# Optimization experiments

Hardware: AMD Instinct MI355X
Metric: run time of the kernel (lower is better)

Reference implementation:

```python
import jax, jax.numpy as jnp
import numpy as np

NEG_SLOPE = 0.2  # PyG GATConv default LeakyReLU slope
BN_EPS = 1e-5


def gat_layer(x, src, dst, W, a_src, a_dst, num_nodes):
    """PyG-style GATConv (no dropout, eval mode). Returns [N, H, C]."""
    H, C = a_src.shape
    h = (x @ W).reshape(-1, H, C)                       # [N,H,C]
    s_src = jnp.einsum('nhc,hc->nh', h, a_src)          # [N,H]
    s_dst = jnp.einsum('nhc,hc->nh', h, a_dst)          # [N,H]
    e = jax.nn.leaky_relu(s_src[src] + s_dst[dst], NEG_SLOPE)  # [E,H]
    # segment softmax over incoming edges of each dst node
    e_max = jax.ops.segment_max(e, dst, num_segments=num_nodes)  # [N,H]
    e_exp = jnp.exp(e - e_max[dst])
    denom = jax.ops.segment_sum(e_exp, dst, num_segments=num_nodes)
    alpha = e_exp / (denom[dst] + 1e-16)                # [E,H]
    msg = h[src] * alpha[:, :, None]                    # [E,H,C] (dominant intermediate)
    return jax.ops.segment_sum(msg, dst, num_segments=num_nodes)  # [N,H,C]


def setup_inputs() -> dict:
    key = jax.random.key(0)
    ks = jax.random.split(key, 12)
    N, Din, Hdim, Heads, Dout = 50000, 128, 128, 8, 128
    E = 150000
    inp = {}
    inp['x'] = jax.random.normal(ks[0], (N, Din), dtype=jnp.float32)
    inp['edge_index'] = jax.random.randint(ks[1], (2, E), 0, N, dtype=jnp.int64)
    sc1 = 1.0 / np.sqrt(Din)
    inp['W1'] = jax.random.uniform(ks[2], (Din, Heads * Hdim), minval=-sc1, maxval=sc1, dtype=jnp.float32)
    inp['a_src1'] = jax.random.normal(ks[3], (Heads, Hdim), dtype=jnp.float32) * 0.1
    inp['a_dst1'] = jax.random.normal(ks[4], (Heads, Hdim), dtype=jnp.float32) * 0.1
    inp['b1'] = jnp.zeros((Heads * Hdim,), dtype=jnp.float32)
    inp['gamma'] = jnp.ones((Heads * Hdim,), dtype=jnp.float32)
    inp['beta'] = jnp.zeros((Heads * Hdim,), dtype=jnp.float32)
    sc2 = 1.0 / np.sqrt(Heads * Hdim)
    inp['W2'] = jax.random.uniform(ks[5], (Heads * Hdim, Dout), minval=-sc2, maxval=sc2, dtype=jnp.float32)
    inp['a_src2'] = jax.random.normal(ks[6], (1, Dout), dtype=jnp.float32) * 0.1
    inp['a_dst2'] = jax.random.normal(ks[7], (1, Dout), dtype=jnp.float32) * 0.1
    inp['b2'] = jnp.zeros((Dout,), dtype=jnp.float32)
    return inp


def reference(x, W1, a_src1, a_dst1, b1, gamma, beta, W2, a_src2, a_dst2, b2, edge_index):
    N = x.shape[0]
    src, dst = edge_index[0], edge_index[1]
    # GAT layer 1: heads=8, concat=True
    h1 = gat_layer(x, src, dst, W1, a_src1, a_dst1, N)   # [N,8,128]
    h1 = h1.reshape(N, -1) + b1                          # [N,1024]
    # BatchNorm1d (training-mode batch stats, biased variance as in torch)
    mu = jnp.mean(h1, axis=0)
    var = jnp.var(h1, axis=0)
    h1 = gamma * (h1 - mu) * jax.lax.rsqrt(var + BN_EPS) + beta
    h1 = jax.nn.elu(h1)
    # GAT layer 2: heads=1, concat=False (mean == squeeze for 1 head)
    h2 = gat_layer(h1, src, dst, W2, a_src2, a_dst2, N)  # [N,1,128]
    return h2[:, 0, :] + b2
```

## Files before the change

kernel.cpp:

```cpp
#include <hip/hip_runtime.h>
#include <hip/hip_bf16.h>
#include <math.h>

#define NEG_SLOPE 0.2f
#define BN_EPS 1e-5f

typedef short bf16x8 __attribute__((ext_vector_type(8)));
typedef float f32x4 __attribute__((ext_vector_type(4)));

__device__ __forceinline__ float bf2f(unsigned short u) {
  union { unsigned int i; float f; } v;
  v.i = ((unsigned int)u) << 16;
  return v.f;
}
__device__ __forceinline__ unsigned short f2bf(float f) {
  union { unsigned int i; float f; } v;
  v.f = f;
  unsigned int i = v.i;
  unsigned int r = (i + 0x7fffu + ((i >> 16) & 1u)) >> 16;
  return (unsigned short)r;
}

__global__ __launch_bounds__(256) void detect_kernel(
    const unsigned int* __restrict__ xw, const unsigned int* __restrict__ eiw,
    int E, int* __restrict__ flags) {
  __shared__ int cnt[2];
  if (threadIdx.x < 2) cnt[threadIdx.x] = 0;
  __syncthreads();
  int t = threadIdx.x;
  int inrange = 0;
  for (int i = t; i < 2048; i += 256) {
    unsigned int e = (xw[i] >> 7) & 0xFFu;
    inrange += (e >= 100u && e <= 135u) ? 1 : 0;
  }
  atomicAdd(&cnt[0], inrange);
  int M = min(1024, E / 2);
  int zeros = 0;
  for (int i = t; i < M; i += 256) zeros += (eiw[2 * i + 1] == 0u) ? 1 : 0;
  atomicAdd(&cnt[1], zeros);
  __syncthreads();
  if (t == 0) {
    flags[0] = (cnt[0] > 1536) ? 1 : 0;
    flags[1] = (cnt[1] > M / 2) ? 1 : 0;
  }
}

__global__ __launch_bounds__(256) void canon_x8(
    const void* __restrict__ src, unsigned short* __restrict__ dst, int n_real,
    int n_total, const int* __restrict__ flags) {
  int i = (blockIdx.x * 256 + threadIdx.x) * 8;
  if (i >= n_total) return;
  union { bf16x8 v; unsigned short u[8]; } o;
  if (i < n_real) {
    if (flags[0]) {
      o.v = *(const bf16x8*)((const unsigned short*)src + i);
    } else {
      const float4* f = (const float4*)((const float*)src + i);
      float4 f0 = f[0];
      float4 f1 = f[1];
      o.u[0] = f2bf(f0.x); o.u[1] = f2bf(f0.y);
      o.u[2] = f2bf(f0.z); o.u[3] = f2bf(f0.w);
      o.u[4] = f2bf(f1.x); o.u[5] = f2bf(f1.y);
      o.u[6] = f2bf(f1.z); o.u[7] = f2bf(f1.w);
    }
  } else {
#pragma unroll
    for (int j = 0; j < 8; ++j) o.u[j] = 0;
  }
  *(bf16x8*)(dst + i) = o.v;
}

__global__ __launch_bounds__(256) void canon_w_t(
    const void* __restrict__ src, unsigned short* __restrict__ dst, int Kdim,
    int Ndim, const int* __restrict__ flags) {
  int i = blockIdx.x * 256 + threadIdx.x;
  if (i >= Kdim * Ndim) return;
  int k = i / Ndim, n = i - k * Ndim;
  unsigned short v = flags[0] ? ((const unsigned short*)src)[i]
                              : f2bf(((const float*)src)[i]);
  dst[(size_t)n * Kdim + k] = v;
}

__global__ __launch_bounds__(1024) void canon_params(
    const void* s0, const void* s1, const void* s2, const void* s3,
    const void* s4, const void* s5, const void* s6, const void* s7,
    unsigned short* d0, unsigned short* d1, unsigned short* d2,
    unsigned short* d3, unsigned short* d4, unsigned short* d5,
    unsigned short* d6, unsigned short* d7, const int* __restrict__ flags) {
  int b = blockIdx.x, t = threadIdx.x;
  const void* s;
  unsigned short* d;
  int n;
  switch (b) {
    case 0: s = s0; d = d0; n = 1024; break;
    case 1: s = s1; d = d1; n = 1024; break;
    case 2: s = s2; d = d2; n = 1024; break;
    case 3: s = s3; d = d3; n = 1024; break;
    case 4: s = s4; d = d4; n = 1024; break;
    case 5: s = s5; d = d5; n = 128; break;
    case 6: s = s6; d = d6; n = 128; break;
    default: s = s7; d = d7; n = 128; break;
  }
  if (t < n)
    d[t] = flags[0] ? ((const unsigned short*)s)[t]
                    : f2bf(((const float*)s)[t]);
}

__global__ __launch_bounds__(256) void canon_idx(
    const int* __restrict__ ei, int* __restrict__ eis, int* __restrict__ eid,
    int E, const int* __restrict__ flags) {
  int e = blockIdx.x * 256 + threadIdx.x;
  if (e >= E) return;
  if (flags[1]) {
    eis[e] = ei[2 * (size_t)e];
    eid[e] = ei[2 * (size_t)E + 2 * (size_t)e];
  } else {
    eis[e] = ei[e];
    eid[e] = ei[E + e];
  }
}

__global__ __launch_bounds__(256) void gemm1_fused(
    const unsigned short* __restrict__ A,
    const unsigned short* __restrict__ Bt,
    unsigned short* __restrict__ C,
    const unsigned short* __restrict__ aScr,
    const unsigned short* __restrict__ aDcr,
    float* __restrict__ ssrc,
    float* __restrict__ sdst,
    int MP) {
  __shared__ unsigned short As[64 * 128];
  __shared__ unsigned short Bs[128 * 128];
  __shared__ float sAll[64][8];
  __shared__ float dAll[64][8];

  const int tid = threadIdx.x;
  const int wid = tid >> 6;
  const int lane = tid & 63;
  const int q = lane >> 4;
  const int r = lane & 15;
  const int wm = wid * 16;
  const int m0 = blockIdx.x * 64;

  const int arow = tid >> 4;
  const int ag = tid & 15;

  bf16x8 ra[4], rb[8];
#pragma unroll
  for (int j = 0; j < 4; ++j)
    ra[j] = *(const bf16x8*)(A + (size_t)(m0 + j * 16 + arow) * 128 + ag * 8);
#pragma unroll
  for (int j = 0; j < 8; ++j)
    rb[j] = *(const bf16x8*)(Bt + (size_t)(j * 16 + arow) * 128 + ag * 8);
#pragma unroll
  for (int j = 0; j < 4; ++j) {
    int row = j * 16 + arow;
    int gs = ag ^ (row & 15);
    *(bf16x8*)(As + row * 128 + gs * 8) = ra[j];
  }
#pragma unroll
  for (int j = 0; j < 8; ++j) {
    int row = j * 16 + arow;
    int gs = ag ^ (row & 15);
    *(bf16x8*)(Bs + row * 128 + gs * 8) = rb[j];
  }
  __syncthreads();

  for (int p = 0; p < 8; ++p) {
    if (p < 7) {
#pragma unroll
      for (int j = 0; j < 8; ++j)
        rb[j] = *(const bf16x8*)(Bt +
                 (size_t)((p + 1) * 128 + j * 16 + arow) * 128 + ag * 8);
    }
    f32x4 acc[8] = {};
#pragma unroll
    for (int ks = 0; ks < 4; ++ks) {
      bf16x8 af = *(const bf16x8*)(As + (wm + r) * 128 +
                                   (((ks * 4 + q) ^ r) << 3));
#pragma unroll
      for (int ni = 0; ni < 8; ++ni) {
        bf16x8 bf = *(const bf16x8*)(Bs + (ni * 16 + r) * 128 +
                                     (((ks * 4 + q) ^ r) << 3));
        acc[ni] = __builtin_amdgcn_mfma_f32_16x16x32_bf16(af, bf, acc[ni],
                                                          0, 0, 0);
      }
    }
#pragma unroll
    for (int ni = 0; ni < 8; ++ni)
#pragma unroll
      for (int i = 0; i < 4; ++i)
        C[(size_t)(m0 + wm + q * 4 + i) * 1024 + p * 128 + ni * 16 + r] =
            f2bf(acc[ni][i]);
    float aSv[8], aDv[8];
#pragma unroll
    for (int ni = 0; ni < 8; ++ni) {
      aSv[ni] = bf2f(aScr[p * 128 + ni * 16 + r]);
      aDv[ni] = bf2f(aDcr[p * 128 + ni * 16 + r]);
    }
#pragma unroll
    for (int i = 0; i < 4; ++i) {
      float ps = 0.f, pd = 0.f;
#pragma unroll
      for (int ni = 0; ni < 8; ++ni) {
        ps += acc[ni][i] * aSv[ni];
        pd += acc[ni][i] * aDv[ni];
      }
      ps += __shfl_xor(ps, 1, 64); pd += __shfl_xor(pd, 1, 64);
      ps += __shfl_xor(ps, 2, 64); pd += __shfl_xor(pd, 2, 64);
      ps += __shfl_xor(ps, 4, 64); pd += __shfl_xor(pd, 4, 64);
      ps += __shfl_xor(ps, 8, 64); pd += __shfl_xor(pd, 8, 64);
      if (r == 0) {
        sAll[wm + q * 4 + i][p] = ps;
        dAll[wm + q * 4 + i][p] = pd;
      }
    }
    __syncthreads();
    if (p < 7) {
#pragma unroll
      for (int j = 0; j < 8; ++j) {
        int row = j * 16 + arow;
        int gs = ag ^ (row & 15);
        *(bf16x8*)(Bs + row * 128 + gs * 8) = rb[j];
      }
      __syncthreads();
    }
  }
  __syncthreads();
  if (tid < 128) {
    float4 v = *((const float4*)&sAll[0][0] + tid);
    *((float4*)(ssrc + (size_t)m0 * 8) + tid) = v;
  } else {
    float4 v = *((const float4*)&dAll[0][0] + (tid - 128));
    *((float4*)(sdst + (size_t)m0 * 8) + (tid - 128)) = v;
  }
}

__global__ __launch_bounds__(256) void gemm2_bn(
    const unsigned short* __restrict__ A,
    const unsigned short* __restrict__ Bt,
    float* __restrict__ C,
    const float* __restrict__ scale, const float* __restrict__ shift,
    const unsigned short* __restrict__ aScr,
    const unsigned short* __restrict__ aDcr,
    float* __restrict__ ssrc, float* __restrict__ sdst) {
  constexpr int K = 1024;
  constexpr int BK = 64;
  constexpr int LDA = BK + 8;
  __shared__ unsigned short As[64 * LDA];
  __shared__ unsigned short Bs[128 * LDA];
  __shared__ float sS[2][64];
  __shared__ float sD[2][64];

  const int m0 = blockIdx.x * 64;
  const int tid = threadIdx.x;
  const int wid = tid >> 6;
  const int lane = tid & 63;
  const int q = lane >> 4;
  const int r = lane & 15;
  const int wm = (wid >> 1) * 32;
  const int wn = (wid & 1) * 64;

  f32x4 acc[2][4] = {};

  const int row0 = tid >> 3;
  const int col0 = (tid & 7) * 8;

  bf16x8 ra[2], rb[4];
#pragma unroll
  for (int ca = 0; ca < 2; ++ca)
    ra[ca] = *(const bf16x8*)(A + (size_t)(m0 + row0 + ca * 32) * K + col0);
#pragma unroll
  for (int cb = 0; cb < 4; ++cb)
    rb[cb] = *(const bf16x8*)(Bt + (size_t)(row0 + cb * 32) * K + col0);

  for (int k0 = 0; k0 < K; k0 += BK) {
    float scv[8], shv[8];
    *(float4*)&scv[0] = *(const float4*)(scale + k0 + col0);
    *(float4*)&scv[4] = *(const float4*)(scale + k0 + col0 + 4);
    *(float4*)&shv[0] = *(const float4*)(shift + k0 + col0);
    *(float4*)&shv[4] = *(const float4*)(shift + k0 + col0 + 4);
#pragma unroll
    for (int ca = 0; ca < 2; ++ca) {
      union { bf16x8 v; unsigned short u[8]; } pk;
      pk.v = ra[ca];
#pragma unroll
      for (int j = 0; j < 8; ++j) {
        float f = bf2f(pk.u[j]) * scv[j] + shv[j];
        f = f > 0.f ? f : (__expf(f) - 1.0f);
        pk.u[j] = f2bf(f);
      }
      *(bf16x8*)(&As[(row0 + ca * 32) * LDA + col0]) = pk.v;
    }
#pragma unroll
    for (int cb = 0; cb < 4; ++cb)
      *(bf16x8*)(&Bs[(row0 + cb * 32) * LDA + col0]) = rb[cb];
    __syncthreads();

    int k1 = k0 + BK;
    if (k1 < K) {
#pragma unroll
      for (int ca = 0; ca < 2; ++ca)
        ra[ca] = *(const bf16x8*)(A + (size_t)(m0 + row0 + ca * 32) * K + k1 +
                                  col0);
#pragma unroll
      for (int cb = 0; cb < 4; ++cb)
        rb[cb] = *(const bf16x8*)(Bt + (size_t)(row0 + cb * 32) * K + k1 +
                                  col0);
    }

#pragma unroll
    for (int ks = 0; ks < BK; ks += 32) {
      bf16x8 af[2], bfv[4];
#pragma unroll
      for (int mi = 0; mi < 2; ++mi)
        af[mi] = *(const bf16x8*)(&As[(wm + mi * 16 + r) * LDA + ks + q * 8]);
#pragma unroll
      for (int ni = 0; ni < 4; ++ni)
        bfv[ni] = *(const bf16x8*)(&Bs[(wn + ni * 16 + r) * LDA + ks + q * 8]);
#pragma unroll
      for (int mi = 0; mi < 2; ++mi)
#pragma unroll
        for (int ni = 0; ni < 4; ++ni)
          acc[mi][ni] = __builtin_amdgcn_mfma_f32_16x16x32_bf16(
              af[mi], bfv[ni], acc[mi][ni], 0, 0, 0);
    }
    __syncthreads();
  }

#pragma unroll
  for (int mi = 0; mi < 2; ++mi)
#pragma unroll
    for (int ni = 0; ni < 4; ++ni)
#pragma unroll
      for (int i = 0; i < 4; ++i) {
        int row = m0 + wm + mi * 16 + q * 4 + i;
        int col = wn + ni * 16 + r;
        C[(size_t)row * 128 + col] = acc[mi][ni][i];
      }

  const int half = wid & 1;
  float aSv[4], aDv[4];
#pragma unroll
  for (int ni = 0; ni < 4; ++ni) {
    aSv[ni] = bf2f(aScr[wn + ni * 16 + r]);
    aDv[ni] = bf2f(aDcr[wn + ni * 16 + r]);
  }
#pragma unroll
  for (int mi = 0; mi < 2; ++mi) {
#pragma unroll
    for (int i = 0; i < 4; ++i) {
      float ps = 0.f, pd = 0.f;
#pragma unroll
      for (int ni = 0; ni < 4; ++ni) {
        float v = acc[mi][ni][i];
        ps += v * aSv[ni];
        pd += v * aDv[ni];
      }
      ps += __shfl_xor(ps, 1, 64); pd += __shfl_xor(pd, 1, 64);
      ps += __shfl_xor(ps, 2, 64); pd += __shfl_xor(pd, 2, 64);
      ps += __shfl_xor(ps, 4, 64); pd += __shfl_xor(pd, 4, 64);
      ps += __shfl_xor(ps, 8, 64); pd += __shfl_xor(pd, 8, 64);
      if (r == 0) {
        int rl = wm + mi * 16 + q * 4 + i;
        sS[half][rl] = ps;
        sD[half][rl] = pd;
      }
    }
  }
  __syncthreads();
  if (tid < 64) {
    ssrc[m0 + tid] = sS[0][tid] + sS[1][tid];
    sdst[m0 + tid] = sD[0][tid] + sD[1][tid];
  }
}

__global__ __launch_bounds__(256) void count_dst(const int* __restrict__ eid,
                                                 int E, int* __restrict__ cnt) {
  int e = blockIdx.x * 256 + threadIdx.x;
  if (e < E) atomicAdd(&cnt[eid[e]], 1);
}

__global__ __launch_bounds__(256) void scan_p1(const int* __restrict__ cnt,
                                               int* __restrict__ bsum, int N) {
  __shared__ int sd[256];
  int b = blockIdx.x, t = threadIdx.x;
  int base = b * 2048;
  int s = 0;
  for (int i = t; i < 2048; i += 256) {
    int idx = base + i;
    if (idx < N) s += cnt[idx];
  }
  sd[t] = s;
  __syncthreads();
  for (int o = 128; o > 0; o >>= 1) {
    if (t < o) sd[t] += sd[t + o];
    __syncthreads();
  }
  if (t == 0) bsum[b] = sd[0];
}

__global__ __launch_bounds__(256) void scan_p2(int* __restrict__ bsum, int nb) {
  __shared__ int sd[256];
  int t = threadIdx.x;
  int own = (t < nb) ? bsum[t] : 0;
  sd[t] = own;
  __syncthreads();
  for (int o = 1; o < 256; o <<= 1) {
    int v = (t >= o) ? sd[t - o] : 0;
    __syncthreads();
    sd[t] += v;
    __syncthreads();
  }
  if (t < nb) bsum[t] = sd[t] - own;
}

__global__ __launch_bounds__(256) void scan_p3(
    const int* __restrict__ cnt, const int* __restrict__ bsum,
    int* __restrict__ offsets, int* __restrict__ cursor, int N) {
  __shared__ int sd[256];
  int b = blockIdx.x, t = threadIdx.x;
  int base = b * 2048 + t * 8;
  int c[8];
  int ts = 0;
#pragma unroll
  for (int j = 0; j < 8; ++j) {
    int idx = base + j;
    c[j] = (idx < N) ? cnt[idx] : 0;
    ts += c[j];
  }
  sd[t] = ts;
  __syncthreads();
  for (int o = 1; o < 256; o <<= 1) {
    int v = (t >= o) ? sd[t - o] : 0;
    __syncthreads();
    sd[t] += v;
    __syncthreads();
  }
  int run = bsum[b] + sd[t] - ts;
#pragma unroll
  for (int j = 0; j < 8; ++j) {
    int idx = base + j;
    if (idx < N) {
      offsets[idx] = run;
      cursor[idx] = run;
      run += c[j];
    }
  }
  if (b == gridDim.x - 1 && t == 255) offsets[N] = bsum[b] + sd[255];
}

__global__ __launch_bounds__(256) void scatter_src(
    const int* __restrict__ eis, const int* __restrict__ eid, int E,
    int* __restrict__ cursor, int* __restrict__ srcs) {
  int e = blockIdx.x * 256 + threadIdx.x;
  if (e >= E) return;
  int d = eid[e];
  int pos = atomicAdd(&cursor[d], 1);
  srcs[pos] = eis[e];
}

__global__ __launch_bounds__(256) void agg1_csr(
    const int* __restrict__ offsets, const int* __restrict__ srcs,
    const unsigned short* __restrict__ h1, const float* __restrict__ ssrc,
    const float* __restrict__ sdst, const unsigned short* __restrict__ b1,
    unsigned short* __restrict__ h1n, int N) {
  int n = blockIdx.x * 4 + (threadIdx.x >> 6);
  if (n >= N) return;
  int lane = threadIdx.x & 63;
  int c0 = lane * 8;
  int c1 = 512 + c0;
  int hA = lane >> 4;
  int beg = offsets[n], end = offsets[n + 1];
  float sdA = sdst[n * 8 + hA];
  float sdB = sdst[n * 8 + hA + 4];
  float accA[8] = {}, accB[8] = {};
  float wsA = 0.f, wsB = 0.f;
  int p = beg;
  for (; p + 2 <= end; p += 2) {
    int s0 = srcs[p], s1 = srcs[p + 1];
    float vA0 = ssrc[s0 * 8 + hA] + sdA;
    float vB0 = ssrc[s0 * 8 + hA + 4] + sdB;
    float vA1 = ssrc[s1 * 8 + hA] + sdA;
    float vB1 = ssrc[s1 * 8 + hA + 4] + sdB;
    union { bf16x8 v; unsigned short u[8]; } uA0, uB0, uA1, uB1;
    uA0.v = *(const bf16x8*)(h1 + (size_t)s0 * 1024 + c0);
    uB0.v = *(const bf16x8*)(h1 + (size_t)s0 * 1024 + c1);
    uA1.v = *(const bf16x8*)(h1 + (size_t)s1 * 1024 + c0);
    uB1.v = *(const bf16x8*)(h1 + (size_t)s1 * 1024 + c1);
    vA0 = vA0 > 0.f ? vA0 : NEG_SLOPE * vA0;
    vB0 = vB0 > 0.f ? vB0 : NEG_SLOPE * vB0;
    vA1 = vA1 > 0.f ? vA1 : NEG_SLOPE * vA1;
    vB1 = vB1 > 0.f ? vB1 : NEG_SLOPE * vB1;
    float wA0 = __expf(vA0), wB0 = __expf(vB0);
    float wA1 = __expf(vA1), wB1 = __expf(vB1);
    wsA += wA0 + wA1;
    wsB += wB0 + wB1;
#pragma unroll
    for (int j = 0; j < 8; ++j) {
      accA[j] = fmaf(bf2f(uA0.u[j]), wA0, accA[j]);
      accB[j] = fmaf(bf2f(uB0.u[j]), wB0, accB[j]);
      accA[j] = fmaf(bf2f(uA1.u[j]), wA1, accA[j]);
      accB[j] = fmaf(bf2f(uB1.u[j]), wB1, accB[j]);
    }
  }
  if (p < end) {
    int s0 = srcs[p];
    float vA0 = ssrc[s0 * 8 + hA] + sdA;
    float vB0 = ssrc[s0 * 8 + hA + 4] + sdB;
    union { bf16x8 v; unsigned short u[8]; } uA0, uB0;
    uA0.v = *(const bf16x8*)(h1 + (size_t)s0 * 1024 + c0);
    uB0.v = *(const bf16x8*)(h1 + (size_t)s0 * 1024 + c1);
    vA0 = vA0 > 0.f ? vA0 : NEG_SLOPE * vA0;
    vB0 = vB0 > 0.f ? vB0 : NEG_SLOPE * vB0;
    float wA0 = __expf(vA0), wB0 = __expf(vB0);
    wsA += wA0;
    wsB += wB0;
#pragma unroll
    for (int j = 0; j < 8; ++j) {
      accA[j] = fmaf(bf2f(uA0.u[j]), wA0, accA[j]);
      accB[j] = fmaf(bf2f(uB0.u[j]), wB0, accB[j]);
    }
  }
  float invA = 1.0f / (wsA + 1e-16f);
  float invB = 1.0f / (wsB + 1e-16f);
  union { bf16x8 v; unsigned short u[8]; } bA, bB, oA, oB;
  bA.v = *(const bf16x8*)(b1 + c0);
  bB.v = *(const bf16x8*)(b1 + c1);
#pragma unroll
  for (int j = 0; j < 8; ++j) {
    oA.u[j] = f2bf(accA[j] * invA + bf2f(bA.u[j]));
    oB.u[j] = f2bf(accB[j] * invB + bf2f(bB.u[j]));
  }
  *(bf16x8*)(h1n + (size_t)n * 1024 + c0) = oA.v;
  *(bf16x8*)(h1n + (size_t)n * 1024 + c1) = oB.v;
}

__global__ __launch_bounds__(256) void bn_stats_part(
    const unsigned short* __restrict__ h1n, float* __restrict__ part, int N,
    int rowsPerBlock) {
  int b = blockIdx.x;
  int half = threadIdx.x >> 7;
  int t = threadIdx.x & 127;
  int c = t * 8;
  int r0 = b * rowsPerBlock;
  int r1 = min(r0 + rowsPerBlock, N);
  float s[8] = {0, 0, 0, 0, 0, 0, 0, 0};
  float q[8] = {0, 0, 0, 0, 0, 0, 0, 0};
  int r = r0 + half;
  for (; r + 2 < r1; r += 4) {
    union { bf16x8 v; unsigned short u[8]; } u0, u1;
    u0.v = *(const bf16x8*)(h1n + (size_t)r * 1024 + c);
    u1.v = *(const bf16x8*)(h1n + (size_t)(r + 2) * 1024 + c);
#pragma unroll
    for (int j = 0; j < 8; ++j) {
      float v0 = bf2f(u0.u[j]);
      float v1 = bf2f(u1.u[j]);
      s[j] += v0 + v1;
      q[j] = fmaf(v0, v0, q[j]);
      q[j] = fmaf(v1, v1, q[j]);
    }
  }
  for (; r < r1; r += 2) {
    union { bf16x8 v; unsigned short u[8]; } u0;
    u0.v = *(const bf16x8*)(h1n + (size_t)r * 1024 + c);
#pragma unroll
    for (int j = 0; j < 8; ++j) {
      float v0 = bf2f(u0.u[j]);
      s[j] += v0;
      q[j] = fmaf(v0, v0, q[j]);
    }
  }
  float* pb = part + ((size_t)b * 2 + half) * 2048;
#pragma unroll
  for (int j = 0; j < 8; ++j) {
    pb[c + j] = s[j];
    pb[1024 + c + j] = q[j];
  }
}

__global__ __launch_bounds__(256) void bn_reduce_finalize(
    const float* __restrict__ part, int nparts,
    const unsigned short* __restrict__ gamma,
    const unsigned short* __restrict__ beta, float* __restrict__ scale,
    float* __restrict__ shift, int N) {
  int c = blockIdx.x * 4 + (threadIdx.x >> 6);
  int lane = threadIdx.x & 63;
  float s = 0.f, q = 0.f;
  for (int b = lane; b < nparts; b += 64) {
    s += part[(size_t)b * 2048 + c];
    q += part[(size_t)b * 2048 + 1024 + c];
  }
#pragma unroll
  for (int o = 32; o > 0; o >>= 1) {
    s += __shfl_xor(s, o, 64);
    q += __shfl_xor(q, o, 64);
  }
  if (lane == 0) {
    float inv_n = 1.0f / (float)N;
    float mu = s * inv_n;
    float var = q * inv_n - mu * mu;
    float sc = bf2f(gamma[c]) * rsqrtf(var + BN_EPS);
    scale[c] = sc;
    shift[c] = bf2f(beta[c]) - mu * sc;
  }
}

__global__ __launch_bounds__(256) void agg2_csr(
    const int* __restrict__ offsets, const int* __restrict__ srcs,
    const float* __restrict__ h2, const float* __restrict__ ssrc,
    const float* __restrict__ sdst, const unsigned short* __restrict__ b2,
    void* __restrict__ out, const int* __restrict__ flags, int N) {
  int n = blockIdx.x * 8 + (threadIdx.x >> 5);
  if (n >= N) return;
  int c = (threadIdx.x & 31) * 4;
  int beg = offsets[n], end = offsets[n + 1];
  float sd = sdst[n];
  float a0 = 0.f, a1 = 0.f, a2 = 0.f, a3 = 0.f, wsum = 0.f;
  int p = beg;
  for (; p + 2 <= end; p += 2) {
    int s0 = srcs[p], s1 = srcs[p + 1];
    float v0 = ssrc[s0] + sd;
    float v1 = ssrc[s1] + sd;
    float4 u0 = *(const float4*)(h2 + (size_t)s0 * 128 + c);
    float4 u1 = *(const float4*)(h2 + (size_t)s1 * 128 + c);
    v0 = v0 > 0.f ? v0 : NEG_SLOPE * v0;
    v1 = v1 > 0.f ? v1 : NEG_SLOPE * v1;
    float w0 = __expf(v0), w1 = __expf(v1);
    wsum += w0 + w1;
    a0 = fmaf(u0.x, w0, a0);
    a1 = fmaf(u0.y, w0, a1);
    a2 = fmaf(u0.z, w0, a2);
    a3 = fmaf(u0.w, w0, a3);
    a0 = fmaf(u1.x, w1, a0);
    a1 = fmaf(u1.y, w1, a1);
    a2 = fmaf(u1.z, w1, a2);
    a3 = fmaf(u1.w, w1, a3);
  }
  if (p < end) {
    int s0 = srcs[p];
    float v0 = ssrc[s0] + sd;
    float4 u0 = *(const float4*)(h2 + (size_t)s0 * 128 + c);
    v0 = v0 > 0.f ? v0 : NEG_SLOPE * v0;
    float w0 = __expf(v0);
    wsum += w0;
    a0 = fmaf(u0.x, w0, a0);
    a1 = fmaf(u0.y, w0, a1);
    a2 = fmaf(u0.z, w0, a2);
    a3 = fmaf(u0.w, w0, a3);
  }
  float inv = 1.0f / (wsum + 1e-16f);
  ushort4 bb = *(const ushort4*)(b2 + c);
  float r0 = a0 * inv + bf2f(bb.x);
  float r1 = a1 * inv + bf2f(bb.y);
  float r2 = a2 * inv + bf2f(bb.z);
  float r3 = a3 * inv + bf2f(bb.w);
  if (flags[0]) {
    ushort4 o;
    o.x = f2bf(r0); o.y = f2bf(r1); o.z = f2bf(r2); o.w = f2bf(r3);
    *(ushort4*)((unsigned short*)out + (size_t)n * 128 + c) = o;
  } else {
    *(float4*)((float*)out + (size_t)n * 128 + c) =
        make_float4(r0, r1, r2, r3);
  }
}

extern "C" void kernel_launch(void* const* d_in, const int* in_sizes, int n_in,
                              void* d_out, int out_size, void* d_ws,
                              size_t ws_size, hipStream_t stream) {
  const void* x      = d_in[0];
  const int*  ei     = (const int*)d_in[1];
  const void* W1     = d_in[2];
  const void* a_src1 = d_in[3];
  const void* a_dst1 = d_in[4];
  const void* b1     = d_in[5];
  const void* gamma  = d_in[6];
  const void* beta   = d_in[7];
  const void* W2     = d_in[8];
  const void* a_src2 = d_in[9];
  const void* a_dst2 = d_in[10];
  const void* b2     = d_in[11];

  const int N = in_sizes[0] / 128;
  const int E = in_sizes[1] / 2;
  const int MP = ((N + 127) / 128) * 128;
  const int NB = (N + 2047) / 2048;
  const int NSTAT = 256;
  const int RPB = (N + NSTAT - 1) / NSTAT;

  char* ws = (char*)d_ws;
  size_t off = 0;
  unsigned short* h1  = (unsigned short*)(ws + off); off += (size_t)MP * 1024 * 2;
  char* h1n_base = ws + off;
  unsigned short* h1n = (unsigned short*)h1n_base;   off += (size_t)MP * 1024 * 2;
  float* ssrc1 = (float*)(ws + off); off += (size_t)MP * 8 * 4;
  float* sdst1 = (float*)(ws + off); off += (size_t)MP * 8 * 4;
  int* offsets = (int*)(ws + off); off += ((size_t)(N + 1) * 4 + 63) & ~63ull;
  int* srcs    = (int*)(ws + off); off += (size_t)E * 4;
  float* part  = (float*)(ws + off); off += (size_t)NSTAT * 2 * 2048 * 4;
  unsigned short* W1t = (unsigned short*)(ws + off); off += 131072 * 2;
  unsigned short* W2t = (unsigned short*)(ws + off); off += 131072 * 2;
  unsigned short* as1c = (unsigned short*)(ws + off); off += 1024 * 2;
  unsigned short* ad1c = (unsigned short*)(ws + off); off += 1024 * 2;
  unsigned short* b1c  = (unsigned short*)(ws + off); off += 1024 * 2;
  unsigned short* gmc  = (unsigned short*)(ws + off); off += 1024 * 2;
  unsigned short* btc  = (unsigned short*)(ws + off); off += 1024 * 2;
  unsigned short* as2c = (unsigned short*)(ws + off); off += 128 * 2;
  unsigned short* ad2c = (unsigned short*)(ws + off); off += 128 * 2;
  unsigned short* b2c  = (unsigned short*)(ws + off); off += 128 * 2;
  float* scale = (float*)(ws + off); off += 1024 * 4;
  float* shift = (float*)(ws + off); off += 1024 * 4;
  int* bsum    = (int*)(ws + off); off += 256 * 4;
  int* flags   = (int*)(ws + off); off += 64;
  unsigned short* x_bf = (unsigned short*)h1n_base;
  int* eis    = (int*)(h1n_base + (16u << 20));
  int* eid    = eis + E;
  int* cnt    = eid + E;
  int* cursor = cnt + N;
  float* h2    = (float*)h1;
  float* ssrc2 = ssrc1;
  float* sdst2 = sdst1;

  detect_kernel<<<1, 256, 0, stream>>>((const unsigned int*)x,
                                       (const unsigned int*)ei, E, flags);
  canon_x8<<<(MP * 128 / 8 + 255) / 256, 256, 0, stream>>>(x, x_bf, N * 128,
                                                           MP * 128, flags);
  canon_w_t<<<(131072 + 255) / 256, 256, 0, stream>>>(W1, W1t, 128, 1024, flags);
  canon_w_t<<<(131072 + 255) / 256, 256, 0, stream>>>(W2, W2t, 1024, 128, flags);
  canon_params<<<8, 1024, 0, stream>>>(a_src1, a_dst1, b1, gamma, beta, a_src2,
                                       a_dst2, b2, as1c, ad1c, b1c, gmc, btc,
                                       as2c, ad2c, b2c, flags);
  canon_idx<<<(E + 255) / 256, 256, 0, stream>>>(ei, eis, eid, E, flags);

  hipMemsetAsync(cnt, 0, (size_t)N * 4, stream);
  hipMemsetAsync((char*)h1n + (size_t)N * 1024 * 2, 0,
                 (size_t)(MP - N) * 1024 * 2, stream);

  count_dst<<<(E + 255) / 256, 256, 0, stream>>>(eid, E, cnt);
  scan_p1<<<NB, 256, 0, stream>>>(cnt, bsum, N);
  scan_p2<<<1, 256, 0, stream>>>(bsum, NB);
  scan_p3<<<NB, 256, 0, stream>>>(cnt, bsum, offsets, cursor, N);
  scatter_src<<<(E + 255) / 256, 256, 0, stream>>>(eis, eid, E, cursor, srcs);

  gemm1_fused<<<MP / 64, 256, 0, stream>>>(x_bf, W1t, h1, as1c, ad1c, ssrc1,
                                           sdst1, MP);
  agg1_csr<<<(N + 3) / 4, 256, 0, stream>>>(offsets, srcs, h1, ssrc1, sdst1,
                                            b1c, h1n, N);

  bn_stats_part<<<NSTAT, 256, 0, stream>>>(h1n, part, N, RPB);
  bn_reduce_finalize<<<256, 256, 0, stream>>>(part, NSTAT * 2, gmc, btc, scale,
                                              shift, N);

  gemm2_bn<<<MP / 64, 256, 0, stream>>>(h1n, W2t, h2, scale, shift, as2c,
                                        ad2c, ssrc2, sdst2);
  agg2_csr<<<(N + 7) / 8, 256, 0, stream>>>(offsets, srcs, h2, ssrc2, sdst2,
                                            b2c, d_out, flags, N);
}
```

Baseline: 349.1 us.

## Fuse x bf16 conversion into gemm1, widen agg2 per-node threads, raise BN partitions

Drops the separate canon_x8 pass and converts x from fp32 to bf16 (or loads it as bf16) directly inside gemm1's A-tile load, zero-filling rows past N. This saves a kernel launch and a write plus re-read of the converted x buffer. agg2 now gives each node a full 64-lane wave, with each lane handling 2 channels instead of 4. The BN stats partition count is doubled to 512 blocks for more parallelism, at the cost of more partials to reduce.

New measurement: 353.8 us. No clear change (+1.4%).

```diff
diff --git a/kernel.cpp b/kernel.cpp
--- a/kernel.cpp
+++ b/kernel.cpp
@@ -43,31 +43,6 @@
     flags[0] = (cnt[0] > 1536) ? 1 : 0;
     flags[1] = (cnt[1] > M / 2) ? 1 : 0;
   }
-}
-
-__global__ __launch_bounds__(256) void canon_x8(
-    const void* __restrict__ src, unsigned short* __restrict__ dst, int n_real,
-    int n_total, const int* __restrict__ flags) {
-  int i = (blockIdx.x * 256 + threadIdx.x) * 8;
-  if (i >= n_total) return;
-  union { bf16x8 v; unsigned short u[8]; } o;
-  if (i < n_real) {
-    if (flags[0]) {
-      o.v = *(const bf16x8*)((const unsigned short*)src + i);
-    } else {
-      const float4* f = (const float4*)((const float*)src + i);
-      float4 f0 = f[0];
-      float4 f1 = f[1];
-      o.u[0] = f2bf(f0.x); o.u[1] = f2bf(f0.y);
-      o.u[2] = f2bf(f0.z); o.u[3] = f2bf(f0.w);
-      o.u[4] = f2bf(f1.x); o.u[5] = f2bf(f1.y);
-      o.u[6] = f2bf(f1.z); o.u[7] = f2bf(f1.w);
-    }
-  } else {
-#pragma unroll
-    for (int j = 0; j < 8; ++j) o.u[j] = 0;
-  }
-  *(bf16x8*)(dst + i) = o.v;
 }
 
 __global__ __launch_bounds__(256) void canon_w_t(
@@ -121,14 +96,14 @@
 }
 
 __global__ __launch_bounds__(256) void gemm1_fused(
-    const unsigned short* __restrict__ A,
+    const void* __restrict__ Araw,
     const unsigned short* __restrict__ Bt,
     unsigned short* __restrict__ C,
     const unsigned short* __restrict__ aScr,
     const unsigned short* __restrict__ aDcr,
     float* __restrict__ ssrc,
     float* __restrict__ sdst,
-    int MP) {
+    int N, int MP, const int* __restrict__ flags) {
   __shared__ unsigned short As[64 * 128];
   __shared__ unsigned short Bs[128 * 128];
   __shared__ float sAll[64][8];
@@ -145,10 +120,33 @@
   const int arow = tid >> 4;
   const int ag = tid & 15;
 
+  const int isbf = flags[0];
+
   bf16x8 ra[4], rb[8];
 #pragma unroll
-  for (int j = 0; j < 4; ++j)
-    ra[j] = *(const bf16x8*)(A + (size_t)(m0 + j * 16 + arow) * 128 + ag * 8);
+  for (int j = 0; j < 4; ++j) {
+    int row = m0 + j * 16 + arow;
+    union { bf16x8 v; unsigned short u[8]; } t;
+    if (row < N) {
+      if (isbf) {
+        t.v = *(const bf16x8*)((const unsigned short*)Araw +
+                               (size_t)row * 128 + ag * 8);
+      } else {
+        const float4* f =
+            (const float4*)((const float*)Araw + (size_t)row * 128 + ag * 8);
+        float4 f0 = f[0];
+        float4 f1 = f[1];
+        t.u[0] = f2bf(f0.x); t.u[1] = f2bf(f0.y);
+        t.u[2] = f2bf(f0.z); t.u[3] = f2bf(f0.w);
+        t.u[4] = f2bf(f1.x); t.u[5] = f2bf(f1.y);
+        t.u[6] = f2bf(f1.z); t.u[7] = f2bf(f1.w);
+      }
+    } else {
+#pragma unroll
+      for (int jj = 0; jj < 8; ++jj) t.u[jj] = 0;
+    }
+    ra[j] = t.v;
+  }
 #pragma unroll
   for (int j = 0; j < 8; ++j)
     rb[j] = *(const bf16x8*)(Bt + (size_t)(j * 16 + arow) * 128 + ag * 8);
@@ -611,57 +609,47 @@
     const float* __restrict__ h2, const float* __restrict__ ssrc,
     const float* __restrict__ sdst, const unsigned short* __restrict__ b2,
     void* __restrict__ out, const int* __restrict__ flags, int N) {
-  int n = blockIdx.x * 8 + (threadIdx.x >> 5);
+  int n = blockIdx.x * 4 + (threadIdx.x >> 6);
   if (n >= N) return;
-  int c = (threadIdx.x & 31) * 4;
+  int c = (threadIdx.x & 63) * 2;
   int beg = offsets[n], end = offsets[n + 1];
   float sd = sdst[n];
-  float a0 = 0.f, a1 = 0.f, a2 = 0.f, a3 = 0.f, wsum = 0.f;
+  float a0 = 0.f, a1 = 0.f, wsum = 0.f;
   int p = beg;
   for (; p + 2 <= end; p += 2) {
     int s0 = srcs[p], s1 = srcs[p + 1];
     float v0 = ssrc[s0] + sd;
     float v1 = ssrc[s1] + sd;
-    float4 u0 = *(const float4*)(h2 + (size_t)s0 * 128 + c);
-    float4 u1 = *(const float4*)(h2 + (size_t)s1 * 128 + c);
+    float2 u0 = *(const float2*)(h2 + (size_t)s0 * 128 + c);
+    float2 u1 = *(const float2*)(h2 + (size_t)s1 * 128 + c);
     v0 = v0 > 0.f ? v0 : NEG_SLOPE * v0;
     v1 = v1 > 0.f ? v1 : NEG_SLOPE * v1;
     float w0 = __expf(v0), w1 = __expf(v1);
     wsum += w0 + w1;
     a0 = fmaf(u0.x, w0, a0);
     a1 = fmaf(u0.y, w0, a1);
-    a2 = fmaf(u0.z, w0, a2);
-    a3 = fmaf(u0.w, w0, a3);
     a0 = fmaf(u1.x, w1, a0);
     a1 = fmaf(u1.y, w1, a1);
-    a2 = fmaf(u1.z, w1, a2);
-    a3 = fmaf(u1.w, w1, a3);
   }
   if (p < end) {
     int s0 = srcs[p];
     float v0 = ssrc[s0] + sd;
-    float4 u0 = *(const float4*)(h2 + (size_t)s0 * 128 + c);
+    float2 u0 = *(const float2*)(h2 + (size_t)s0 * 128 + c);
     v0 = v0 > 0.f ? v0 : NEG_SLOPE * v0;
     float w0 = __expf(v0);
     wsum += w0;
     a0 = fmaf(u0.x, w0, a0);
     a1 = fmaf(u0.y, w0, a1);
-    a2 = fmaf(u0.z, w0, a2);
-    a3 = fmaf(u0.w, w0, a3);
   }
   float inv = 1.0f / (wsum + 1e-16f);
-  ushort4 bb = *(const ushort4*)(b2 + c);
-  float r0 = a0 * inv + bf2f(bb.x);
-  float r1 = a1 * inv + bf2f(bb.y);
-  float r2 = a2 * inv + bf2f(bb.z);
-  float r3 = a3 * inv + bf2f(bb.w);
+  unsigned int bb = *(const unsigned int*)(b2 + c);
+  float r0 = a0 * inv + bf2f(bb & 0xffff);
+  float r1 = a1 * inv + bf2f(bb >> 16);
   if (flags[0]) {
-    ushort4 o;
-    o.x = f2bf(r0); o.y = f2bf(r1); o.z = f2bf(r2); o.w = f2bf(r3);
-    *(ushort4*)((unsigned short*)out + (size_t)n * 128 + c) = o;
+    unsigned int o = (unsigned int)f2bf(r0) | ((unsigned int)f2bf(r1) << 16);
+    *(unsigned int*)((unsigned short*)out + (size_t)n * 128 + c) = o;
   } else {
-    *(float4*)((float*)out + (size_t)n * 128 + c) =
-        make_float4(r0, r1, r2, r3);
+    *(float2*)((float*)out + (size_t)n * 128 + c) = make_float2(r0, r1);
   }
 }
 
@@ -685,7 +673,7 @@
   const int E = in_sizes[1] / 2;
   const int MP = ((N + 127) / 128) * 128;
   const int NB = (N + 2047) / 2048;
-  const int NSTAT = 256;
+  const int NSTAT = 512;
   const int RPB = (N + NSTAT - 1) / NSTAT;
 
   char* ws = (char*)d_ws;
@@ -712,7 +700,6 @@
   float* shift = (float*)(ws + off); off += 1024 * 4;
   int* bsum    = (int*)(ws + off); off += 256 * 4;
   int* flags   = (int*)(ws + off); off += 64;
-  unsigned short* x_bf = (unsigned short*)h1n_base;
   int* eis    = (int*)(h1n_base + (16u << 20));
   int* eid    = eis + E;
   int* cnt    = eid + E;
@@ -723,8 +710,6 @@
 
   detect_kernel<<<1, 256, 0, stream>>>((const unsigned int*)x,
                                        (const unsigned int*)ei, E, flags);
-  canon_x8<<<(MP * 128 / 8 + 255) / 256, 256, 0, stream>>>(x, x_bf, N * 128,
-                                                           MP * 128, flags);
   canon_w_t<<<(131072 + 255) / 256, 256, 0, stream>>>(W1, W1t, 128, 1024, flags);
   canon_w_t<<<(131072 + 255) / 256, 256, 0, stream>>>(W2, W2t, 1024, 128, flags);
   canon_params<<<8, 1024, 0, stream>>>(a_src1, a_dst1, b1, gamma, beta, a_src2,
@@ -742,8 +727,8 @@
   scan_p3<<<NB, 256, 0, stream>>>(cnt, bsum, offsets, cursor, N);
   scatter_src<<<(E + 255) / 256, 256, 0, stream>>>(eis, eid, E, cursor, srcs);
 
-  gemm1_fused<<<MP / 64, 256, 0, stream>>>(x_bf, W1t, h1, as1c, ad1c, ssrc1,
-                                           sdst1, MP);
+  gemm1_fused<<<MP / 64, 256, 0, stream>>>(x, W1t, h1, as1c, ad1c, ssrc1,
+                                           sdst1, N, MP, flags);
   agg1_csr<<<(N + 3) / 4, 256, 0, stream>>>(offsets, srcs, h1, ssrc1, sdst1,
                                             b1c, h1n, N);
 
@@ -753,6 +738,6 @@
 
   gemm2_bn<<<MP / 64, 256, 0, stream>>>(h1n, W2t, h2, scale, shift, as2c,
                                         ad2c, ssrc2, sdst2);
-  agg2_csr<<<(N + 7) / 8, 256, 0, stream>>>(offsets, srcs, h2, ssrc2, sdst2,
+  agg2_csr<<<(N + 3) / 4, 256, 0, stream>>>(offsets, srcs, h2, ssrc2, sdst2,
                                             b2c, d_out, flags, N);
 }
```
